# Kernel optimization log

Hardware: AMD Instinct MI355X
Metric: run time of the kernel (lower is better)

The kernel has to match this reference:

```python
import jax, jax.numpy as jnp
import numpy as np

B, S, F, E, R, O = 4, 2048, 2048, 16, 16, 2048
TEMPERATURE = 1.0


def setup_inputs() -> dict:
    key = jax.random.key(0)
    k1, k2, k3, k4 = jax.random.split(key, 4)
    x = jax.random.normal(k1, (B, S, F), dtype=jnp.float32)
    prototypes = jax.random.normal(k2, (E, F), dtype=jnp.float32)
    # prototypes are top right-singular vectors -> unit norm rows
    prototypes = prototypes / jnp.linalg.norm(prototypes, axis=1, keepdims=True)
    A_stack = jax.random.normal(k3, (E, R, F), dtype=jnp.float32) * 0.02
    B_stack = jax.random.normal(k4, (E, O, R), dtype=jnp.float32) * 0.02
    scaling = jnp.float32(2.0)
    return {"x": x, "prototypes": prototypes, "A_stack": A_stack,
            "B_stack": B_stack, "scaling": scaling, "top_k": 4}


def reference(x, prototypes, A_stack, B_stack, scaling, top_k):
    lead = x.shape[:-1]
    f_in = x.shape[-1]
    tok = x.reshape(-1, f_in)                       # (t, F)
    t = tok.shape[0]

    # Arrow routing: abs cosine-like similarity to per-expert prototypes
    sim = jnp.abs(tok @ prototypes.T)               # (t, E)
    top_v, idx = jax.lax.top_k(sim, top_k)          # (t, k)
    full_score = jnp.full(sim.shape, -jnp.inf, dtype=sim.dtype)
    full_score = full_score.at[jnp.arange(t)[:, None], idx].set(top_v)
    coeff = jax.nn.softmax(full_score / TEMPERATURE, axis=1)  # (t, E), zeros off top-k

    # Per-expert LoRA: z = tok @ A_e^T  (dense over all experts, as in source)
    z = jnp.einsum('tf,erf->ter', tok, A_stack)     # (t, E, r)
    # Combine coeff into the low-rank space before the B projection to avoid
    # materializing the (t, E, out) tensor; math identical to
    # einsum('te, teo -> to', coeff, einsum('ter,eor->teo', z, B_stack)).
    delta = jnp.einsum('te,ter,eor->to', coeff, z, B_stack)  # (t, O)

    delta = scaling * delta                          # dropout = identity (eval)
    return delta.reshape(lead + (delta.shape[-1],))
```

## Files before the change

kernel.cpp:

```cpp
#include <hip/hip_runtime.h>
#include <hip/hip_bf16.h>
#include <stdint.h>

#define T_TOKENS 8192
#define F_DIM    2048
#define E_EXP    16
#define R_RANK   16
#define O_DIM    2048
#define KDIM     (E_EXP * R_RANK)

typedef short v8s __attribute__((ext_vector_type(8)));
typedef float v4f __attribute__((ext_vector_type(4)));

#define AS1 __attribute__((address_space(1)))
#define AS3 __attribute__((address_space(3)))

__device__ __forceinline__ uint16_t f2bf(float f) {
  uint32_t u = __builtin_bit_cast(uint32_t, f);
  u += 0x7fffu + ((u >> 16) & 1u);
  return (uint16_t)(u >> 16);
}

__device__ __forceinline__ void g2lds16(const uint16_t* g, uint16_t* l) {
  __builtin_amdgcn_global_load_lds((AS1 void*)g, (AS3 void*)l, 16, 0, 0);
}

__global__ __launch_bounds__(256) void route_stream(
    const float* __restrict__ x, const float* __restrict__ P,
    const float* __restrict__ A, const float* __restrict__ Bst,
    uint16_t* __restrict__ xb, float4* __restrict__ partials4,
    uint16_t* __restrict__ Ab, uint16_t* __restrict__ Bb) {
  __shared__ float ps[16 * 260];
  const int tid = threadIdx.x;
  const int c   = blockIdx.x;
  const int by  = blockIdx.y;

  if (by >= 128) {
    const int gid = ((by - 128) * 8 + c) * 256 + tid;
    for (int i = gid; i < KDIM * F_DIM; i += 64 * 256)
      Ab[i] = f2bf(A[i]);
    for (int i = gid; i < O_DIM * KDIM; i += 64 * 256) {
      const int k = i & (KDIM - 1);
      const int o = i >> 8;
      const int e = k >> 4, r = k & 15;
      Bb[i] = f2bf(Bst[((size_t)e * O_DIM + o) * R_RANK + r]);
    }
    return;
  }

  const int f0 = c * 256;
  {
    const int e = tid >> 4;
    #pragma unroll
    for (int j = 0; j < 4; ++j) {
      const int col = (tid & 15) * 4 + j * 64;
      *(float4*)&ps[e * 260 + col] =
          *(const float4*)&P[(size_t)e * F_DIM + f0 + col];
    }
  }
  __syncthreads();

  const int sub = tid & 15;
  const int tg  = tid >> 4;
  const int t0  = by * 64 + tg * 4;
  const float* xr = x + (size_t)t0 * F_DIM + f0;
  uint16_t*    xw = xb + (size_t)t0 * F_DIM + f0;

  float a0[16], a1[16], a2[16], a3[16];
  #pragma unroll
  for (int e = 0; e < 16; ++e) { a0[e] = 0.f; a1[e] = 0.f; a2[e] = 0.f; a3[e] = 0.f; }

  #pragma unroll
  for (int j = 0; j < 4; ++j) {
    const int off = sub * 4 + j * 64;
    float4 v0 = *(const float4*)&xr[off];
    float4 v1 = *(const float4*)&xr[F_DIM + off];
    float4 v2 = *(const float4*)&xr[2 * F_DIM + off];
    float4 v3 = *(const float4*)&xr[3 * F_DIM + off];
    uint2 p0, p1, p2, p3;
    p0.x = (uint32_t)f2bf(v0.x) | ((uint32_t)f2bf(v0.y) << 16);
    p0.y = (uint32_t)f2bf(v0.z) | ((uint32_t)f2bf(v0.w) << 16);
    p1.x = (uint32_t)f2bf(v1.x) | ((uint32_t)f2bf(v1.y) << 16);
    p1.y = (uint32_t)f2bf(v1.z) | ((uint32_t)f2bf(v1.w) << 16);
    p2.x = (uint32_t)f2bf(v2.x) | ((uint32_t)f2bf(v2.y) << 16);
    p2.y = (uint32_t)f2bf(v2.z) | ((uint32_t)f2bf(v2.w) << 16);
    p3.x = (uint32_t)f2bf(v3.x) | ((uint32_t)f2bf(v3.y) << 16);
    p3.y = (uint32_t)f2bf(v3.z) | ((uint32_t)f2bf(v3.w) << 16);
    *(uint2*)&xw[off]             = p0;
    *(uint2*)&xw[F_DIM + off]     = p1;
    *(uint2*)&xw[2 * F_DIM + off] = p2;
    *(uint2*)&xw[3 * F_DIM + off] = p3;
    #pragma unroll
    for (int e = 0; e < 16; ++e) {
      float4 pv = *(float4*)&ps[e * 260 + off];
      a0[e] += v0.x * pv.x; a0[e] += v0.y * pv.y; a0[e] += v0.z * pv.z; a0[e] += v0.w * pv.w;
      a1[e] += v1.x * pv.x; a1[e] += v1.y * pv.y; a1[e] += v1.z * pv.z; a1[e] += v1.w * pv.w;
      a2[e] += v2.x * pv.x; a2[e] += v2.y * pv.y; a2[e] += v2.z * pv.z; a2[e] += v2.w * pv.w;
      a3[e] += v3.x * pv.x; a3[e] += v3.y * pv.y; a3[e] += v3.z * pv.z; a3[e] += v3.w * pv.w;
    }
  }

  #pragma unroll
  for (int e = 0; e < 16; ++e) {
    #pragma unroll
    for (int m = 1; m < 16; m <<= 1) {
      a0[e] += __shfl_xor(a0[e], m, 64);
      a1[e] += __shfl_xor(a1[e], m, 64);
      a2[e] += __shfl_xor(a2[e], m, 64);
      a3[e] += __shfl_xor(a3[e], m, 64);
    }
  }

  const size_t cb = (size_t)c * 4;
  if (sub == 0) {
    #pragma unroll
    for (int e4 = 0; e4 < 4; ++e4)
      partials4[(cb + e4) * T_TOKENS + t0] =
          make_float4(a0[e4 * 4], a0[e4 * 4 + 1], a0[e4 * 4 + 2], a0[e4 * 4 + 3]);
  } else if (sub == 1) {
    #pragma unroll
    for (int e4 = 0; e4 < 4; ++e4)
      partials4[(cb + e4) * T_TOKENS + t0 + 1] =
          make_float4(a1[e4 * 4], a1[e4 * 4 + 1], a1[e4 * 4 + 2], a1[e4 * 4 + 3]);
  } else if (sub == 2) {
    #pragma unroll
    for (int e4 = 0; e4 < 4; ++e4)
      partials4[(cb + e4) * T_TOKENS + t0 + 2] =
          make_float4(a2[e4 * 4], a2[e4 * 4 + 1], a2[e4 * 4 + 2], a2[e4 * 4 + 3]);
  } else if (sub == 3) {
    #pragma unroll
    for (int e4 = 0; e4 < 4; ++e4)
      partials4[(cb + e4) * T_TOKENS + t0 + 3] =
          make_float4(a3[e4 * 4], a3[e4 * 4 + 1], a3[e4 * 4 + 2], a3[e4 * 4 + 3]);
  }
}

__global__ __launch_bounds__(256) void gemm_xa(
    const uint16_t* __restrict__ xb, const uint16_t* __restrict__ Ab,
    const float4* __restrict__ partials4, const float* __restrict__ scaling,
    const int* __restrict__ topk, uint16_t* __restrict__ wb) {
  __shared__ uint16_t S[16384];
  __shared__ float coeffL[64 * 17];
  uint16_t* X0 = S;
  uint16_t* X1 = S + 4096;
  uint16_t* A0 = S + 8192;
  uint16_t* A1 = S + 12288;
  const int tid  = threadIdx.x;
  const int b    = blockIdx.x;
  const int m_idx = (b & 7) + ((b >> 5) << 3);
  const int n_idx = (b >> 3) & 3;
  const int m0 = m_idx * 64, n0 = n_idx * 64;
  const int lane = tid & 63;
  const int wid  = tid >> 6;
  const int wm   = (wid >> 1) * 32;
  const int wn   = (wid & 1) * 32;
  const int quad = lane >> 4;
  const int cl   = lane & 15;

  const int G0 = wid * 64 + lane;
  const int G1 = G0 + 256;
  const int r0 = G0 >> 3, g0 = (G0 & 7) ^ (r0 & 7);
  const int r1 = G1 >> 3, g1 = (G1 & 7) ^ (r1 & 7);
  const uint16_t* xs0 = xb + (size_t)(m0 + r0) * F_DIM + g0 * 8;
  const uint16_t* xs1 = xb + (size_t)(m0 + r1) * F_DIM + g1 * 8;
  const uint16_t* as0 = Ab + (size_t)(n0 + r0) * F_DIM + g0 * 8;
  const uint16_t* as1 = Ab + (size_t)(n0 + r1) * F_DIM + g1 * 8;
  const int d0 = wid * 512;
  const int d1 = wid * 512 + 2048;

  const int ma0 = wm + cl, ma1 = wm + 16 + cl;
  const int nb0 = wn + cl, nb1 = wn + 16 + cl;

#define STAGE_XA(Xb_, Ab_, kk) do {       \
    g2lds16(xs0 + (kk), (Xb_) + d0);      \
    g2lds16(xs1 + (kk), (Xb_) + d1);      \
    g2lds16(as0 + (kk), (Ab_) + d0);      \
    g2lds16(as1 + (kk), (Ab_) + d1);      \
  } while (0)

#define COMP_XA(Xb_, Ab_) do {                                                            \
    _Pragma("unroll")                                                                     \
    for (int ks = 0; ks < 2; ++ks) {                                                      \
      const int gk = ks * 4 + quad;                                                       \
      v8s fa0 = *(v8s*)&(Xb_)[(ma0 * 8 + (gk ^ (ma0 & 7))) * 8];                          \
      v8s fa1 = *(v8s*)&(Xb_)[(ma1 * 8 + (gk ^ (ma1 & 7))) * 8];                          \
      v8s fb0 = *(v8s*)&(Ab_)[(nb0 * 8 + (gk ^ (nb0 & 7))) * 8];                          \
      v8s fb1 = *(v8s*)&(Ab_)[(nb1 * 8 + (gk ^ (nb1 & 7))) * 8];                          \
      acc[0][0] = __builtin_amdgcn_mfma_f32_16x16x32_bf16(fa0, fb0, acc[0][0], 0, 0, 0);  \
      acc[0][1] = __builtin_amdgcn_mfma_f32_16x16x32_bf16(fa0, fb1, acc[0][1], 0, 0, 0);  \
      acc[1][0] = __builtin_amdgcn_mfma_f32_16x16x32_bf16(fa1, fb0, acc[1][0], 0, 0, 0);  \
      acc[1][1] = __builtin_amdgcn_mfma_f32_16x16x32_bf16(fa1, fb1, acc[1][1], 0, 0, 0);  \
    }                                                                                     \
  } while (0)

  v4f acc[2][2];
  #pragma unroll
  for (int i = 0; i < 2; i++)
    #pragma unroll
    for (int j = 0; j < 2; j++) acc[i][j] = (v4f){0.f, 0.f, 0.f, 0.f};

  STAGE_XA(X0, A0, 0);

  if (tid < 64) {
    const int t = m0 + tid;
    double s[16];
    #pragma unroll
    for (int e = 0; e < 16; ++e) s[e] = 0.0;
    for (int c = 0; c < 8; ++c) {
      #pragma unroll
      for (int e4 = 0; e4 < 4; ++e4) {
        float4 p = partials4[((size_t)c * 4 + e4) * T_TOKENS + t];
        s[e4 * 4]     += (double)p.x;
        s[e4 * 4 + 1] += (double)p.y;
        s[e4 * 4 + 2] += (double)p.z;
        s[e4 * 4 + 3] += (double)p.w;
      }
    }
    double v[16];
    #pragma unroll
    for (int e = 0; e < 16; ++e) v[e] = fabs(s[e]);
    int k = topk[0];
    if (k > 16) k = 16;
    if (k < 1)  k = 1;
    unsigned mask = 0;
    double mx = 0.0;
    float ssum = 0.f;
    for (int i = 0; i < k; ++i) {
      double bv = -1.0; int bj = 0;
      #pragma unroll
      for (int j = 0; j < 16; ++j) {
        bool ok = !((mask >> j) & 1u) && (v[j] > bv);
        bv = ok ? v[j] : bv;
        bj = ok ? j  : bj;
      }
      mask |= 1u << bj;
      if (i == 0) mx = bv;
      ssum += expf((float)(bv - mx));
    }
    const float sc = scaling[0];
    #pragma unroll
    for (int j = 0; j < 16; ++j)
      coeffL[tid * 17 + j] = ((mask >> j) & 1u)
          ? expf((float)(v[j] - mx)) / ssum * sc : 0.f;
  }

  for (int k0 = 0; k0 < F_DIM; k0 += 128) {
    __syncthreads();
    STAGE_XA(X1, A1, k0 + 64);
    COMP_XA(X0, A0);
    __syncthreads();
    if (k0 + 128 < F_DIM) STAGE_XA(X0, A0, k0 + 128);
    COMP_XA(X1, A1);
  }

  __syncthreads();
  uint16_t* tile = S;
  #pragma unroll
  for (int mi = 0; mi < 2; mi++)
    #pragma unroll
    for (int ni = 0; ni < 2; ni++) {
      const int nl = wn + ni * 16 + cl;
      const int eidx = (n0 + nl) >> 4;
      #pragma unroll
      for (int reg = 0; reg < 4; reg++) {
        const int tl = wm + mi * 16 + quad * 4 + reg;
        float wv = acc[mi][ni][reg] * coeffL[tl * 17 + eidx];
        tile[tl * 72 + nl] = f2bf(wv);
      }
    }
  __syncthreads();
  #pragma unroll
  for (int p = 0; p < 2; ++p) {
    const int row  = p * 32 + (tid >> 3);
    const int colg = (tid & 7) * 8;
    uint4 val = *(uint4*)&tile[row * 72 + colg];
    *(uint4*)&wb[(size_t)(m0 + row) * KDIM + n0 + colg] = val;
  }
#undef STAGE_XA
#undef COMP_XA
}

__global__ __launch_bounds__(256) void gemm_wb(
    const uint16_t* __restrict__ wbuf, const uint16_t* __restrict__ Bb,
    float* __restrict__ out) {
  __shared__ uint16_t S[20480];
  uint16_t* Ws = S;
  uint16_t* Bs = S + 4096;
  const int tid  = threadIdx.x;
  const int b    = blockIdx.x;
  const int m_idx = (b & 7) + ((b >> 6) << 3);
  const int n_idx = (b >> 3) & 7;
  const int m0 = m_idx * 64;
  const int n0 = n_idx * 256;
  const int lane = tid & 63;
  const int wid  = tid >> 6;
  const int wm   = (wid >> 1) * 32;
  const int wn   = (wid & 1) * 128;
  const int quad = lane >> 4;
  const int cl   = lane & 15;

  const int GW0 = wid * 64 + lane;
  const int GW1 = GW0 + 256;
  const int wr0 = GW0 >> 3, wg0 = (GW0 & 7) ^ (wr0 & 7);
  const int wr1 = GW1 >> 3, wg1 = (GW1 & 7) ^ (wr1 & 7);
  const uint16_t* wsrc0 = wbuf + (size_t)(m0 + wr0) * KDIM + wg0 * 8;
  const uint16_t* wsrc1 = wbuf + (size_t)(m0 + wr1) * KDIM + wg1 * 8;

  const uint16_t* bsrc[8];
  #pragma unroll
  for (int p = 0; p < 8; ++p) {
    const int G = p * 256 + wid * 64 + lane;
    const int r = G >> 3, g = (G & 7) ^ (r & 7);
    bsrc[p] = Bb + (size_t)(n0 + r) * KDIM + g * 8;
  }

  v4f acc[2][8];
  #pragma unroll
  for (int i = 0; i < 2; i++)
    #pragma unroll
    for (int j = 0; j < 8; j++) acc[i][j] = (v4f){0.f, 0.f, 0.f, 0.f};

  const int ma0 = wm + cl, ma1 = wm + 16 + cl;

  #pragma unroll
  for (int k0 = 0; k0 < KDIM; k0 += 64) {
    __syncthreads();
    g2lds16(wsrc0 + k0, Ws + wid * 512);
    g2lds16(wsrc1 + k0, Ws + wid * 512 + 2048);
    #pragma unroll
    for (int p = 0; p < 8; ++p)
      g2lds16(bsrc[p] + k0, Bs + (p * 256 + wid * 64) * 8);
    __syncthreads();
    #pragma unroll
    for (int ks = 0; ks < 2; ++ks) {
      const int gk = ks * 4 + quad;
      v8s fa0 = *(v8s*)&Ws[(ma0 * 8 + (gk ^ (ma0 & 7))) * 8];
      v8s fa1 = *(v8s*)&Ws[(ma1 * 8 + (gk ^ (ma1 & 7))) * 8];
      v8s fb[8];
      #pragma unroll
      for (int j = 0; j < 8; ++j) {
        const int nb = wn + j * 16 + cl;
        fb[j] = *(v8s*)&Bs[(nb * 8 + (gk ^ (nb & 7))) * 8];
      }
      #pragma unroll
      for (int j = 0; j < 8; ++j) {
        acc[0][j] = __builtin_amdgcn_mfma_f32_16x16x32_bf16(fa0, fb[j], acc[0][j], 0, 0, 0);
        acc[1][j] = __builtin_amdgcn_mfma_f32_16x16x32_bf16(fa1, fb[j], acc[1][j], 0, 0, 0);
      }
    }
  }

  float* ft = (float*)S;
  #pragma unroll
  for (int h = 0; h < 2; ++h) {
    __syncthreads();
    if ((wid >> 1) == h) {
      #pragma unroll
      for (int mi = 0; mi < 2; mi++)
        #pragma unroll
        for (int j = 0; j < 8; j++) {
          const int col = wn + j * 16 + cl;
          #pragma unroll
          for (int reg = 0; reg < 4; reg++) {
            const int rl = mi * 16 + quad * 4 + reg;
            ft[rl * 260 + col] = acc[mi][j][reg];
          }
        }
    }
    __syncthreads();
    #pragma unroll
    for (int p = 0; p < 8; ++p) {
      const int f4  = p * 256 + tid;
      const int row = f4 >> 6;
      const int c4  = f4 & 63;
      float4 v = *(float4*)&ft[row * 260 + c4 * 4];
      *(float4*)&out[(size_t)(m0 + h * 32 + row) * O_DIM + n0 + c4 * 4] = v;
    }
  }
}

extern "C" void kernel_launch(void* const* d_in, const int* in_sizes, int n_in,
                              void* d_out, int out_size, void* d_ws, size_t ws_size,
                              hipStream_t stream) {
  (void)in_sizes; (void)n_in; (void)out_size; (void)ws_size;
  const float* x       = (const float*)d_in[0];
  const float* P       = (const float*)d_in[1];
  const float* A       = (const float*)d_in[2];
  const float* Bst     = (const float*)d_in[3];
  const float* scaling = (const float*)d_in[4];
  const int*   topk    = (const int*)d_in[5];
  float* out = (float*)d_out;

  char* ws = (char*)d_ws;
  uint16_t* xb     = (uint16_t*)(ws);
  uint16_t* Ab     = (uint16_t*)(ws + 33554432);
  uint16_t* Bb     = (uint16_t*)(ws + 34603008);
  uint16_t* wbuf   = (uint16_t*)(ws + 35651584);
  float4*   parts  = (float4*)  (ws + 39845888);

  hipLaunchKernelGGL(route_stream, dim3(8, 136), dim3(256), 0, stream,
                     x, P, A, Bst, xb, parts, Ab, Bb);
  hipLaunchKernelGGL(gemm_xa, dim3(512), dim3(256), 0, stream,
                     xb, Ab, parts, scaling, topk, wbuf);
  hipLaunchKernelGGL(gemm_wb, dim3(1024), dim3(256), 0, stream, wbuf, Bb, out);
}
```

Baseline: 179.5 us.

## Split weight conversion into own kernel, widen routing F-chunks, prefetch x rows

Moves the A/B bf16 conversion out of route_stream into a separate prep_weights kernel. route_stream now handles 512-wide F chunks (4 column blocks instead of 8), which halves the routing partials to reduce, and it software-prefetches the next x float4s. gemm_xa spreads the routing top-k/softmax across four waves (one lane per token per wave) instead of only the first 64 threads. This adds one kernel launch and lowers route_stream's grid parallelism, and the larger prefetch state raises register pressure.

```diff
diff --git a/kernel.cpp b/kernel.cpp
--- a/kernel.cpp
+++ b/kernel.cpp
@@ -25,36 +25,36 @@
   __builtin_amdgcn_global_load_lds((AS1 void*)g, (AS3 void*)l, 16, 0, 0);
 }
 
+__global__ __launch_bounds__(256) void prep_weights(
+    const float* __restrict__ A, const float* __restrict__ Bst,
+    uint16_t* __restrict__ Ab, uint16_t* __restrict__ Bb) {
+  int idx = blockIdx.x * 256 + threadIdx.x;
+  if (idx < KDIM * F_DIM) {
+    Ab[idx] = f2bf(A[idx]);
+  }
+  if (idx < O_DIM * KDIM) {
+    int k = idx & (KDIM - 1);
+    int o = idx >> 8;
+    int e = k >> 4, r = k & 15;
+    Bb[idx] = f2bf(Bst[((size_t)e * O_DIM + o) * R_RANK + r]);
+  }
+}
+
 __global__ __launch_bounds__(256) void route_stream(
     const float* __restrict__ x, const float* __restrict__ P,
-    const float* __restrict__ A, const float* __restrict__ Bst,
-    uint16_t* __restrict__ xb, float4* __restrict__ partials4,
-    uint16_t* __restrict__ Ab, uint16_t* __restrict__ Bb) {
-  __shared__ float ps[16 * 260];
+    uint16_t* __restrict__ xb, float4* __restrict__ partials4) {
+  __shared__ float ps[16 * 516];
   const int tid = threadIdx.x;
   const int c   = blockIdx.x;
   const int by  = blockIdx.y;
-
-  if (by >= 128) {
-    const int gid = ((by - 128) * 8 + c) * 256 + tid;
-    for (int i = gid; i < KDIM * F_DIM; i += 64 * 256)
-      Ab[i] = f2bf(A[i]);
-    for (int i = gid; i < O_DIM * KDIM; i += 64 * 256) {
-      const int k = i & (KDIM - 1);
-      const int o = i >> 8;
-      const int e = k >> 4, r = k & 15;
-      Bb[i] = f2bf(Bst[((size_t)e * O_DIM + o) * R_RANK + r]);
-    }
-    return;
-  }
-
-  const int f0 = c * 256;
+  const int f0  = c * 512;
+
   {
     const int e = tid >> 4;
     #pragma unroll
-    for (int j = 0; j < 4; ++j) {
+    for (int j = 0; j < 8; ++j) {
       const int col = (tid & 15) * 4 + j * 64;
-      *(float4*)&ps[e * 260 + col] =
+      *(float4*)&ps[e * 516 + col] =
           *(const float4*)&P[(size_t)e * F_DIM + f0 + col];
     }
   }
@@ -70,13 +70,23 @@
   #pragma unroll
   for (int e = 0; e < 16; ++e) { a0[e] = 0.f; a1[e] = 0.f; a2[e] = 0.f; a3[e] = 0.f; }
 
-  #pragma unroll
-  for (int j = 0; j < 4; ++j) {
+  const int off0 = sub * 4;
+  float4 v0 = *(const float4*)&xr[off0];
+  float4 v1 = *(const float4*)&xr[F_DIM + off0];
+  float4 v2 = *(const float4*)&xr[2 * F_DIM + off0];
+  float4 v3 = *(const float4*)&xr[3 * F_DIM + off0];
+
+  #pragma unroll
+  for (int j = 0; j < 8; ++j) {
     const int off = sub * 4 + j * 64;
-    float4 v0 = *(const float4*)&xr[off];
-    float4 v1 = *(const float4*)&xr[F_DIM + off];
-    float4 v2 = *(const float4*)&xr[2 * F_DIM + off];
-    float4 v3 = *(const float4*)&xr[3 * F_DIM + off];
+    float4 n0, n1, n2, n3;
+    if (j < 7) {
+      const int offn = off + 64;
+      n0 = *(const float4*)&xr[offn];
+      n1 = *(const float4*)&xr[F_DIM + offn];
+      n2 = *(const float4*)&xr[2 * F_DIM + offn];
+      n3 = *(const float4*)&xr[3 * F_DIM + offn];
+    }
     uint2 p0, p1, p2, p3;
     p0.x = (uint32_t)f2bf(v0.x) | ((uint32_t)f2bf(v0.y) << 16);
     p0.y = (uint32_t)f2bf(v0.z) | ((uint32_t)f2bf(v0.w) << 16);
@@ -92,12 +102,13 @@
     *(uint2*)&xw[3 * F_DIM + off] = p3;
     #pragma unroll
     for (int e = 0; e < 16; ++e) {
-      float4 pv = *(float4*)&ps[e * 260 + off];
+      float4 pv = *(float4*)&ps[e * 516 + off];
       a0[e] += v0.x * pv.x; a0[e] += v0.y * pv.y; a0[e] += v0.z * pv.z; a0[e] += v0.w * pv.w;
       a1[e] += v1.x * pv.x; a1[e] += v1.y * pv.y; a1[e] += v1.z * pv.z; a1[e] += v1.w * pv.w;
       a2[e] += v2.x * pv.x; a2[e] += v2.y * pv.y; a2[e] += v2.z * pv.z; a2[e] += v2.w * pv.w;
       a3[e] += v3.x * pv.x; a3[e] += v3.y * pv.y; a3[e] += v3.z * pv.z; a3[e] += v3.w * pv.w;
     }
+    v0 = n0; v1 = n1; v2 = n2; v3 = n3;
   }
 
   #pragma unroll
@@ -201,12 +212,14 @@
 
   STAGE_XA(X0, A0, 0);
 
-  if (tid < 64) {
-    const int t = m0 + tid;
+  if (cl == lane) {
+    const int tk = wid * 16 + cl;
+    const int t  = m0 + tk;
     double s[16];
     #pragma unroll
     for (int e = 0; e < 16; ++e) s[e] = 0.0;
-    for (int c = 0; c < 8; ++c) {
+    #pragma unroll
+    for (int c = 0; c < 4; ++c) {
       #pragma unroll
       for (int e4 = 0; e4 < 4; ++e4) {
         float4 p = partials4[((size_t)c * 4 + e4) * T_TOKENS + t];
@@ -240,7 +253,7 @@
     const float sc = scaling[0];
     #pragma unroll
     for (int j = 0; j < 16; ++j)
-      coeffL[tid * 17 + j] = ((mask >> j) & 1u)
+      coeffL[tk * 17 + j] = ((mask >> j) & 1u)
           ? expf((float)(v[j] - mx)) / ssum * sc : 0.f;
   }
 
@@ -398,8 +411,8 @@
   uint16_t* wbuf   = (uint16_t*)(ws + 35651584);
   float4*   parts  = (float4*)  (ws + 39845888);
 
-  hipLaunchKernelGGL(route_stream, dim3(8, 136), dim3(256), 0, stream,
-                     x, P, A, Bst, xb, parts, Ab, Bb);
+  hipLaunchKernelGGL(prep_weights, dim3(2048), dim3(256), 0, stream, A, Bst, Ab, Bb);
+  hipLaunchKernelGGL(route_stream, dim3(4, 128), dim3(256), 0, stream, x, P, xb, parts);
   hipLaunchKernelGGL(gemm_xa, dim3(512), dim3(256), 0, stream,
                      xb, Ab, parts, scaling, topk, wbuf);
   hipLaunchKernelGGL(gemm_wb, dim3(1024), dim3(256), 0, stream, wbuf, Bb, out);
```

New measurement: 182.6 us. About the same (+1.7%).
